# Optimization experiments

Measured on AMD Instinct MI355X. Metric: run time of the kernel, lower is better.

Reference implementation:

```python
import jax, jax.numpy as jnp
import numpy as np

N, H, V = 8192, 1024, 32000
IGNORE_INDEX = -100
LABEL_SMOOTHING = 0.0
LOGIT_SCALE = 1.0


def setup_inputs() -> dict:
    key = jax.random.key(0)
    k1, k2, k3 = jax.random.split(key, 3)
    x = jax.random.normal(k1, (N, H), dtype=jnp.float32)
    weight = jax.random.normal(k2, (V, H), dtype=jnp.float32) * 0.02
    bias = jnp.zeros((V,), dtype=jnp.float32)
    target = jax.random.randint(k3, (N,), 0, V, dtype=jnp.int64)
    return {"x": x, "weight": weight, "bias": bias, "target": target}


def reference(x, weight, bias, target):
    # logits: [N, V]; fused kernel never materializes this fully, but math is identical
    logits = (x @ weight.T + bias) * LOGIT_SCALE
    lse = jax.nn.logsumexp(logits.astype(jnp.float32), axis=-1)  # [N]
    valid = target != IGNORE_INDEX
    safe_t = jnp.where(valid, target, 0)
    tgt_logit = jnp.take_along_axis(logits, safe_t[:, None], axis=-1)[:, 0]
    loss_i = lse - tgt_logit
    if LABEL_SMOOTHING > 0:
        eps = LABEL_SMOOTHING / V
        z = (-eps * logits).sum(-1)
        loss_i = loss_i * (1.0 - LABEL_SMOOTHING) + (z + LABEL_SMOOTHING * lse)
    loss_i = jnp.where(valid, loss_i, 0.0)
    total = jnp.maximum(valid.sum(), 1)
    # reduction == 'mean': each per-token loss divided by total, then summed
    return loss_i.sum() / total
```

## Files before the change

kernel.cpp:

```cpp
#include <hip/hip_runtime.h>
#include <math.h>

typedef int    intx8    __attribute__((ext_vector_type(8)));
typedef float  floatx16 __attribute__((ext_vector_type(16)));

#define N_ROWS 8192
#define H_DIM  1024
#define V_DIM  32000
#define V_PAD  32768
#define IGNORE_INDEX (-100)

#define S_SPLITS 16
#define TILES_PER_SPLIT 16
#define BM 256
#define BN 128
#define KSTEPS 16
#define TOTAL_STEPS (TILES_PER_SPLIT * KSTEPS)
#define BBUF (4 * 128 * 16)

#define LOG2E 1.4426950408889634f
#define LN2   0.6931471805599453f

__global__ __launch_bounds__(256) void convert_fp8(const float* __restrict__ in,
                                                   unsigned char* __restrict__ out,
                                                   int Rstride, float scale) {
  const int r = blockIdx.x * 256 + threadIdx.x;
  const int u = blockIdx.y;
  const float4* src = (const float4*)(in + (size_t)r * H_DIM + u * 16);
  uint4 res;
#pragma unroll
  for (int j = 0; j < 4; ++j) {
    const float4 v = src[j];
    int p = __builtin_amdgcn_cvt_pk_fp8_f32(v.x * scale, v.y * scale, 0, false);
    p = __builtin_amdgcn_cvt_pk_fp8_f32(v.z * scale, v.w * scale, p, true);
    ((int*)&res)[j] = p;
  }
  *(uint4*)(out + ((size_t)u * Rstride + r) * 16) = res;
}

__global__ __launch_bounds__(256) void pad_bias(const float* __restrict__ bias,
                                                float* __restrict__ biasp) {
  const int i = blockIdx.x * 256 + threadIdx.x;
  biasp[i] = (i < V_DIM) ? bias[i] * LOG2E : -1e30f;
}


typedef union { intx8 v; uint4 q[2]; } afrag;

#define BDMA(T) do {                                                                     \
    const int _t = (T);                                                                  \
    const int _ub = (_t & 15) * 4;                                                       \
    const int _n0 = (sidx * TILES_PER_SPLIT + (_t >> 4)) * BN;                           \
    unsigned char* _d = smB + ((_t & 1) ? BBUF : 0);                                     \
    _Pragma("unroll")                                                                    \
    for (int _j = 0; _j < 2; ++_j) {                                                     \
      const int _c = _j * 4 + w, _u = _c >> 1, _rb = _c & 1;                             \
      __builtin_amdgcn_global_load_lds(                                                  \
          (const __attribute__((address_space(1))) void*)(wsb +                          \
              ((size_t)(_ub + _u) * V_PAD + _n0 + _rb * 64 + lane) * 16),                \
          (__attribute__((address_space(3))) void*)(_d + ((_u * 128 + _rb * 64 + lane) * 16)), \
          16, 0, 0);                                                                     \
    }                                                                                    \
  } while (0)

#define ALD(T, DST) do {                                                                 \
    const int _u2 = ((T) & 15) * 4 + half * 2;                                           \
    DST[0].q[0] = *(const uint4*)(xs + (((size_t)(_u2    ) * N_ROWS + arow0) * 16));     \
    DST[0].q[1] = *(const uint4*)(xs + (((size_t)(_u2 + 1) * N_ROWS + arow0) * 16));     \
    DST[1].q[0] = *(const uint4*)(xs + (((size_t)(_u2    ) * N_ROWS + arow1) * 16));     \
    DST[1].q[1] = *(const uint4*)(xs + (((size_t)(_u2 + 1) * N_ROWS + arow1) * 16));     \
  } while (0)

#define STEP(T, AU, AL) do {                                                             \
    const int _st = (T);                                                                 \
    __syncthreads();       \
    if (_st + 1 < TOTAL_STEPS) {                                                         \
      BDMA(_st + 1);                                                                     \
      ALD(_st + 1, AL);                                                                  \
    }                                                                                    \
    const unsigned char* _pB = smB + ((_st & 1) ? BBUF : 0);                             \
    afrag b[4];                                                                          \
    const int _ua = half * 2;                                                            \
    _Pragma("unroll")                                                                    \
    for (int nb = 0; nb < 4; ++nb) {                                                     \
      b[nb].q[0] = *(const uint4*)(_pB + ((_ua * 128 + nb * 32 + l31) * 16));            \
      b[nb].q[1] = *(const uint4*)(_pB + (((_ua + 1) * 128 + nb * 32 + l31) * 16));      \
    }                                                                                    \
    __builtin_amdgcn_s_setprio(1);                                                       \
    _Pragma("unroll")                                                                    \
    for (int mb = 0; mb < 2; ++mb)                                                       \
      _Pragma("unroll")                                                                  \
      for (int nb = 0; nb < 4; ++nb)                                                     \
        acc[mb][nb] = __builtin_amdgcn_mfma_scale_f32_32x32x64_f8f6f4(                   \
            AU[mb].v, b[nb].v, acc[mb][nb],                                              \
            0, 0,                                                  \
            0, 0x7F7F7F7F,                                            \
            0, 0x7F7F7F7F);                                           \
    __builtin_amdgcn_s_setprio(0);                                                       \
  } while (0)

__global__ __launch_bounds__(256, 2) void flce_main(const unsigned char* __restrict__ xs,
                                                    const unsigned char* __restrict__ wsb,
                                                    const float* __restrict__ biasp,
                                                    float* __restrict__ partials) {
  __shared__ __align__(16) unsigned char smB[2 * BBUF];

  const int tid  = threadIdx.x;
  const int lane = tid & 63;
  const int w    = tid >> 6;
  const int l31  = lane & 31;
  const int half = lane >> 5;
  const int wr   = w * 64;

  const int hw     = blockIdx.y * 32 + blockIdx.x;
  const int rowblk = hw >> 4;
  const int sidx   = ((hw & 7) << 1) | ((hw >> 3) & 1);
  const int row0   = rowblk * BM;

  const size_t arow0 = (size_t)(row0 + wr + l31);
  const size_t arow1 = arow0 + 32;

  float l_state[32];
#pragma unroll
  for (int i = 0; i < 32; ++i) l_state[i] = 0.f;

  afrag aE[2], aO[2];

  BDMA(0);
  ALD(0, aE);

#pragma unroll 1
  for (int ct = 0; ct < TILES_PER_SPLIT; ++ct) {
    floatx16 acc[2][4];
#pragma unroll
    for (int mb = 0; mb < 2; ++mb)
#pragma unroll
      for (int nb = 0; nb < 4; ++nb)
#pragma unroll
        for (int i = 0; i < 16; ++i) acc[mb][nb][i] = 0.f;

#pragma unroll 1
    for (int ks2 = 0; ks2 < 8; ++ks2) {
      const int st0 = ct * KSTEPS + ks2 * 2;
      STEP(st0,     aE, aO);
      STEP(st0 + 1, aO, aE);
    }

    const int n0 = (sidx * TILES_PER_SPLIT + ct) * BN;
    float bnb[4];
#pragma unroll
    for (int nb = 0; nb < 4; ++nb) bnb[nb] = biasp[n0 + nb * 32 + l31];
#pragma unroll
    for (int mb = 0; mb < 2; ++mb)
#pragma unroll
      for (int r = 0; r < 16; ++r) {
        float s = exp2f(acc[mb][0][r] + bnb[0]) + exp2f(acc[mb][1][r] + bnb[1])
                + exp2f(acc[mb][2][r] + bnb[2]) + exp2f(acc[mb][3][r] + bnb[3]);
        l_state[mb * 16 + r] += s;
      }
  }

#pragma unroll
  for (int s = 0; s < 32; ++s) {
    float v = l_state[s];
#pragma unroll
    for (int off = 1; off < 32; off <<= 1) v += __shfl_xor(v, off, 64);
    l_state[s] = v;
  }

  if (l31 == 0) {
#pragma unroll
    for (int s = 0; s < 32; ++s) {
      const int mb = s >> 4, r = s & 15;
      const int row = wr + mb * 32 + 4 * half + (r & 3) + 8 * (r >> 2);
      partials[(size_t)(row0 + row) * S_SPLITS + sidx] = l_state[s];
    }
  }
}

__global__ __launch_bounds__(256) void tgt_kernel(const float* __restrict__ x,
                                                  const float* __restrict__ wgt,
                                                  const float* __restrict__ bias,
                                                  const int* __restrict__ target,
                                                  float* __restrict__ tgt_logit) {
  const int r = blockIdx.x * 4 + (threadIdx.x >> 6);
  const int lane = threadIdx.x & 63;
  const int t = target[r];
  const int tt = (t == IGNORE_INDEX) ? 0 : t;
  const float4* xr = (const float4*)(x + (size_t)r * H_DIM);
  const float4* wr = (const float4*)(wgt + (size_t)tt * H_DIM);
  float acc = 0.f;
#pragma unroll
  for (int i = 0; i < 4; ++i) {
    const float4 a = xr[lane + i * 64];
    const float4 b = wr[lane + i * 64];
    acc += a.x * b.x + a.y * b.y + a.z * b.z + a.w * b.w;
  }
#pragma unroll
  for (int off = 32; off >= 1; off >>= 1) acc += __shfl_xor(acc, off, 64);
  if (lane == 0) tgt_logit[r] = acc + bias[tt];
}

__global__ __launch_bounds__(256) void loss_rows(const float* __restrict__ partials,
                                                 const float* __restrict__ tgt_logit,
                                                 const int* __restrict__ target,
                                                 float* __restrict__ bsums) {
  const int r = blockIdx.x * 256 + threadIdx.x;
  float l = 0.f;
#pragma unroll
  for (int s = 0; s < S_SPLITS; ++s) l += partials[(size_t)r * S_SPLITS + s];
  const float lse = LN2 * __log2f(l);
  const bool valid = (target[r] != IGNORE_INDEX);
  float loss = valid ? (lse - tgt_logit[r]) : 0.f;
  float cnt  = valid ? 1.f : 0.f;
  const int lane = threadIdx.x & 63;
  const int w = threadIdx.x >> 6;
#pragma unroll
  for (int off = 32; off >= 1; off >>= 1) {
    loss += __shfl_xor(loss, off, 64);
    cnt  += __shfl_xor(cnt, off, 64);
  }
  __shared__ float sl[4], sc[4];
  if (lane == 0) { sl[w] = loss; sc[w] = cnt; }
  __syncthreads();
  if (threadIdx.x == 0) {
    float S = 0.f, C = 0.f;
    for (int i = 0; i < 4; ++i) { S += sl[i]; C += sc[i]; }
    bsums[blockIdx.x] = S;
    bsums[32 + blockIdx.x] = C;
  }
}

__global__ void finalize(const float* __restrict__ bsums, float* __restrict__ out) {
  const int t = threadIdx.x;
  float s = (t < 32) ? bsums[t] : 0.f;
  float c = (t < 32) ? bsums[32 + t] : 0.f;
#pragma unroll
  for (int off = 32; off >= 1; off >>= 1) {
    s += __shfl_xor(s, off, 64);
    c += __shfl_xor(c, off, 64);
  }
  if (t == 0) out[0] = s / fmaxf(c, 1.f);
}

extern "C" void kernel_launch(void* const* d_in, const int* in_sizes, int n_in,
                              void* d_out, int out_size, void* d_ws, size_t ws_size,
                              hipStream_t stream) {
  const float* x    = (const float*)d_in[0];
  const float* wgt  = (const float*)d_in[1];
  const float* bias = (const float*)d_in[2];
  const int*   tgt  = (const int*)d_in[3];
  float* out = (float*)d_out;

  char* ws = (char*)d_ws;
  const size_t XS8 = (size_t)N_ROWS * H_DIM;
  const size_t WS8 = (size_t)V_PAD * H_DIM;
  const size_t BP  = (size_t)V_PAD * 4;
  const size_t PB  = (size_t)N_ROWS * S_SPLITS * 4;
  unsigned char* xs8 = (unsigned char*)ws;
  unsigned char* ws8 = (unsigned char*)(ws + XS8);
  float* biasp    = (float*)(ws + XS8 + WS8);
  float* partials = (float*)(ws + XS8 + WS8 + BP);
  float* tgt_lg   = (float*)(ws + XS8 + WS8 + BP + PB);
  float* bsums    = (float*)(ws + XS8 + WS8 + BP + PB + (size_t)N_ROWS * 4);

  convert_fp8<<<dim3(N_ROWS / 256, H_DIM / 16), 256, 0, stream>>>(x, xs8, N_ROWS, LOG2E);
  convert_fp8<<<dim3(V_DIM / 256, H_DIM / 16), 256, 0, stream>>>(wgt, ws8, V_PAD, 1.0f);
  pad_bias<<<V_PAD / 256, 256, 0, stream>>>(bias, biasp);
  tgt_kernel<<<N_ROWS / 4, 256, 0, stream>>>(x, wgt, bias, tgt, tgt_lg);
  flce_main<<<dim3(N_ROWS / BM, S_SPLITS), 256, 0, stream>>>(xs8, ws8, biasp, partials);
  loss_rows<<<N_ROWS / 256, 256, 0, stream>>>(partials, tgt_lg, tgt, bsums);
  finalize<<<1, 64, 0, stream>>>(bsums, out);
}
```

Baseline: 555.0 us.

## Deepen K-step to 128, split MFMA halves around barrier, stage bias in LDS

The main GEMM loop now handles two 64-wide K chunks per step. The B tile buffer is doubled, and the A fragment for the next step is loaded between the two MFMA halves, with a mid-step barrier, so load latency overlaps compute. Per-tile bias values are preloaded into LDS once by async copy instead of read from global memory each tile. The block-index swizzle is replaced with plain grid mapping. The fp8 convert kernel is also remapped so each thread reads contiguous row chunks for better coalescing, at the cost of more LDS use and a possible loss of L2 locality from dropping the swizzle.

```diff
diff --git a/kernel.cpp b/kernel.cpp
--- a/kernel.cpp
+++ b/kernel.cpp
@@ -14,9 +14,9 @@
 #define TILES_PER_SPLIT 16
 #define BM 256
 #define BN 128
-#define KSTEPS 16
+#define KSTEPS 8
 #define TOTAL_STEPS (TILES_PER_SPLIT * KSTEPS)
-#define BBUF (4 * 128 * 16)
+#define BBUF (8 * 128 * 16)
 
 #define LOG2E 1.4426950408889634f
 #define LN2   0.6931471805599453f
@@ -24,9 +24,9 @@
 __global__ __launch_bounds__(256) void convert_fp8(const float* __restrict__ in,
                                                    unsigned char* __restrict__ out,
                                                    int Rstride, float scale) {
-  const int r = blockIdx.x * 256 + threadIdx.x;
-  const int u = blockIdx.y;
-  const float4* src = (const float4*)(in + (size_t)r * H_DIM + u * 16);
+  const int row = blockIdx.x * 4 + (threadIdx.x >> 6);
+  const int u   = threadIdx.x & 63;
+  const float4* src = (const float4*)(in + (size_t)row * H_DIM + u * 16);
   uint4 res;
 #pragma unroll
   for (int j = 0; j < 4; ++j) {
@@ -35,7 +35,7 @@
     p = __builtin_amdgcn_cvt_pk_fp8_f32(v.z * scale, v.w * scale, p, true);
     ((int*)&res)[j] = p;
   }
-  *(uint4*)(out + ((size_t)u * Rstride + r) * 16) = res;
+  *(uint4*)(out + ((size_t)u * Rstride + row) * 16) = res;
 }
 
 __global__ __launch_bounds__(256) void pad_bias(const float* __restrict__ bias,
@@ -45,58 +45,85 @@
 }
 
 
-typedef union { intx8 v; uint4 q[2]; } afrag;
+typedef union { intx8 v; uint4 q[2]; } frag;
 
 #define BDMA(T) do {                                                                     \
     const int _t = (T);                                                                  \
-    const int _ub = (_t & 15) * 4;                                                       \
-    const int _n0 = (sidx * TILES_PER_SPLIT + (_t >> 4)) * BN;                           \
+    const int _tub = (_t & 7) * 8;                                                       \
+    const int _n0 = (sidx * TILES_PER_SPLIT + (_t >> 3)) * BN;                           \
     unsigned char* _d = smB + ((_t & 1) ? BBUF : 0);                                     \
     _Pragma("unroll")                                                                    \
-    for (int _j = 0; _j < 2; ++_j) {                                                     \
+    for (int _j = 0; _j < 4; ++_j) {                                                     \
       const int _c = _j * 4 + w, _u = _c >> 1, _rb = _c & 1;                             \
       __builtin_amdgcn_global_load_lds(                                                  \
           (const __attribute__((address_space(1))) void*)(wsb +                          \
-              ((size_t)(_ub + _u) * V_PAD + _n0 + _rb * 64 + lane) * 16),                \
+              ((size_t)(_tub + _u) * V_PAD + _n0 + _rb * 64 + lane) * 16),               \
           (__attribute__((address_space(3))) void*)(_d + ((_u * 128 + _rb * 64 + lane) * 16)), \
           16, 0, 0);                                                                     \
     }                                                                                    \
   } while (0)
 
-#define ALD(T, DST) do {                                                                 \
-    const int _u2 = ((T) & 15) * 4 + half * 2;                                           \
-    DST[0].q[0] = *(const uint4*)(xs + (((size_t)(_u2    ) * N_ROWS + arow0) * 16));     \
-    DST[0].q[1] = *(const uint4*)(xs + (((size_t)(_u2 + 1) * N_ROWS + arow0) * 16));     \
-    DST[1].q[0] = *(const uint4*)(xs + (((size_t)(_u2    ) * N_ROWS + arow1) * 16));     \
-    DST[1].q[1] = *(const uint4*)(xs + (((size_t)(_u2 + 1) * N_ROWS + arow1) * 16));     \
-  } while (0)
-
-#define STEP(T, AU, AL) do {                                                             \
+#define STEP(T, AK0, AK0N) do {                                                          \
     const int _st = (T);                                                                 \
-    __syncthreads();       \
+    const int _ub = (_st & 7) * 8;                                                       \
+    __syncthreads();            \
+                                 \
+                 \
+    frag aK1[2];                                                                         \
+    {                                                                                    \
+      const size_t _u1 = (size_t)(_ub + 4 + half2);                                      \
+      aK1[0].q[0] = *(const uint4*)(xs + ((_u1 * N_ROWS + arow0) * 16));                 \
+      aK1[0].q[1] = *(const uint4*)(xs + (((_u1 + 1) * N_ROWS + arow0) * 16));           \
+      aK1[1].q[0] = *(const uint4*)(xs + ((_u1 * N_ROWS + arow1) * 16));                 \
+      aK1[1].q[1] = *(const uint4*)(xs + (((_u1 + 1) * N_ROWS + arow1) * 16));           \
+    }                                                                                    \
+    if (_st + 1 < TOTAL_STEPS) BDMA(_st + 1);           \
+    const unsigned char* _pB = smB + ((_st & 1) ? BBUF : 0);                             \
+           \
+    {                                                                                    \
+      frag b[4];                                                                         \
+      _Pragma("unroll")                                                                  \
+      for (int nb = 0; nb < 4; ++nb) {                                                   \
+        b[nb].q[0] = *(const uint4*)(_pB + (((half2    ) * 128 + nb * 32 + l31) * 16));  \
+        b[nb].q[1] = *(const uint4*)(_pB + (((half2 + 1) * 128 + nb * 32 + l31) * 16));  \
+      }                                                                                  \
+      __builtin_amdgcn_s_setprio(1);                                                     \
+      _Pragma("unroll")                                                                  \
+      for (int mb = 0; mb < 2; ++mb)                                                     \
+        _Pragma("unroll")                                                                \
+        for (int nb = 0; nb < 4; ++nb)                                                   \
+          acc[mb][nb] = __builtin_amdgcn_mfma_scale_f32_32x32x64_f8f6f4(                 \
+              AK0[mb].v, b[nb].v, acc[mb][nb],                                           \
+              0, 0, 0, 0x7F7F7F7F, 0, 0x7F7F7F7F);                                       \
+      __builtin_amdgcn_s_setprio(0);                                                     \
+    }                                                                                    \
+    __builtin_amdgcn_s_barrier();         \
+                                   \
     if (_st + 1 < TOTAL_STEPS) {                                                         \
-      BDMA(_st + 1);                                                                     \
-      ALD(_st + 1, AL);                                                                  \
-    }                                                                                    \
-    const unsigned char* _pB = smB + ((_st & 1) ? BBUF : 0);                             \
-    afrag b[4];                                                                          \
-    const int _ua = half * 2;                                                            \
-    _Pragma("unroll")                                                                    \
-    for (int nb = 0; nb < 4; ++nb) {                                                     \
-      b[nb].q[0] = *(const uint4*)(_pB + ((_ua * 128 + nb * 32 + l31) * 16));            \
-      b[nb].q[1] = *(const uint4*)(_pB + (((_ua + 1) * 128 + nb * 32 + l31) * 16));      \
-    }                                                                                    \
-    __builtin_amdgcn_s_setprio(1);                                                       \
-    _Pragma("unroll")                                                                    \
-    for (int mb = 0; mb < 2; ++mb)                                                       \
+      const size_t _u0 = (size_t)((((_st + 1) & 7) * 8) + half2);                        \
+      AK0N[0].q[0] = *(const uint4*)(xs + ((_u0 * N_ROWS + arow0) * 16));                \
+      AK0N[0].q[1] = *(const uint4*)(xs + (((_u0 + 1) * N_ROWS + arow0) * 16));          \
+      AK0N[1].q[0] = *(const uint4*)(xs + ((_u0 * N_ROWS + arow1) * 16));                \
+      AK0N[1].q[1] = *(const uint4*)(xs + (((_u0 + 1) * N_ROWS + arow1) * 16));          \
+    }                                                                                    \
+                      \
+    {                                                                                    \
+      frag b[4];                                                                         \
       _Pragma("unroll")                                                                  \
-      for (int nb = 0; nb < 4; ++nb)                                                     \
-        acc[mb][nb] = __builtin_amdgcn_mfma_scale_f32_32x32x64_f8f6f4(                   \
-            AU[mb].v, b[nb].v, acc[mb][nb],                                              \
-            0, 0,                                                  \
-            0, 0x7F7F7F7F,                                            \
-            0, 0x7F7F7F7F);                                           \
-    __builtin_amdgcn_s_setprio(0);                                                       \
+      for (int nb = 0; nb < 4; ++nb) {                                                   \
+        b[nb].q[0] = *(const uint4*)(_pB + (((4 + half2) * 128 + nb * 32 + l31) * 16));  \
+        b[nb].q[1] = *(const uint4*)(_pB + (((5 + half2) * 128 + nb * 32 + l31) * 16));  \
+      }                                                                                  \
+      __builtin_amdgcn_s_setprio(1);                                                     \
+      _Pragma("unroll")                                                                  \
+      for (int mb = 0; mb < 2; ++mb)                                                     \
+        _Pragma("unroll")                                                                \
+        for (int nb = 0; nb < 4; ++nb)                                                   \
+          acc[mb][nb] = __builtin_amdgcn_mfma_scale_f32_32x32x64_f8f6f4(                 \
+              aK1[mb].v, b[nb].v, acc[mb][nb],                                           \
+              0, 0, 0, 0x7F7F7F7F, 0, 0x7F7F7F7F);                                       \
+      __builtin_amdgcn_s_setprio(0);                                                     \
+    }                                                                                    \
   } while (0)
 
 __global__ __launch_bounds__(256, 2) void flce_main(const unsigned char* __restrict__ xs,
@@ -104,18 +131,17 @@
                                                     const float* __restrict__ biasp,
                                                     float* __restrict__ partials) {
   __shared__ __align__(16) unsigned char smB[2 * BBUF];
+  __shared__ __align__(16) float sbias[TILES_PER_SPLIT * BN];
 
   const int tid  = threadIdx.x;
   const int lane = tid & 63;
   const int w    = tid >> 6;
   const int l31  = lane & 31;
   const int half = lane >> 5;
+  const int half2 = half * 2;
   const int wr   = w * 64;
-
-  const int hw     = blockIdx.y * 32 + blockIdx.x;
-  const int rowblk = hw >> 4;
-  const int sidx   = ((hw & 7) << 1) | ((hw >> 3) & 1);
-  const int row0   = rowblk * BM;
+  const int row0 = blockIdx.x * BM;
+  const int sidx = blockIdx.y;
 
   const size_t arow0 = (size_t)(row0 + wr + l31);
   const size_t arow1 = arow0 + 32;
@@ -124,10 +150,24 @@
 #pragma unroll
   for (int i = 0; i < 32; ++i) l_state[i] = 0.f;
 
-  afrag aE[2], aO[2];
-
+#pragma unroll
+  for (int j = 0; j < 2; ++j) {
+    const int c = j * 4 + w;
+    __builtin_amdgcn_global_load_lds(
+        (const __attribute__((address_space(1))) void*)(biasp +
+            (size_t)sidx * (TILES_PER_SPLIT * BN) + c * 256 + lane * 4),
+        (__attribute__((address_space(3))) void*)(sbias + c * 256 + lane * 4),
+        16, 0, 0);
+  }
   BDMA(0);
-  ALD(0, aE);
+  frag aK0E[2], aK0O[2];
+  {
+    const size_t _u0 = (size_t)half2;
+    aK0E[0].q[0] = *(const uint4*)(xs + ((_u0 * N_ROWS + arow0) * 16));
+    aK0E[0].q[1] = *(const uint4*)(xs + (((_u0 + 1) * N_ROWS + arow0) * 16));
+    aK0E[1].q[0] = *(const uint4*)(xs + ((_u0 * N_ROWS + arow1) * 16));
+    aK0E[1].q[1] = *(const uint4*)(xs + (((_u0 + 1) * N_ROWS + arow1) * 16));
+  }
 
 #pragma unroll 1
   for (int ct = 0; ct < TILES_PER_SPLIT; ++ct) {
@@ -140,16 +180,15 @@
         for (int i = 0; i < 16; ++i) acc[mb][nb][i] = 0.f;
 
 #pragma unroll 1
-    for (int ks2 = 0; ks2 < 8; ++ks2) {
+    for (int ks2 = 0; ks2 < 4; ++ks2) {
       const int st0 = ct * KSTEPS + ks2 * 2;
-      STEP(st0,     aE, aO);
-      STEP(st0 + 1, aO, aE);
+      STEP(st0,     aK0E, aK0O);
+      STEP(st0 + 1, aK0O, aK0E);
     }
 
-    const int n0 = (sidx * TILES_PER_SPLIT + ct) * BN;
     float bnb[4];
 #pragma unroll
-    for (int nb = 0; nb < 4; ++nb) bnb[nb] = biasp[n0 + nb * 32 + l31];
+    for (int nb = 0; nb < 4; ++nb) bnb[nb] = sbias[ct * BN + nb * 32 + l31];
 #pragma unroll
     for (int mb = 0; mb < 2; ++mb)
 #pragma unroll
@@ -264,8 +303,8 @@
   float* tgt_lg   = (float*)(ws + XS8 + WS8 + BP + PB);
   float* bsums    = (float*)(ws + XS8 + WS8 + BP + PB + (size_t)N_ROWS * 4);
 
-  convert_fp8<<<dim3(N_ROWS / 256, H_DIM / 16), 256, 0, stream>>>(x, xs8, N_ROWS, LOG2E);
-  convert_fp8<<<dim3(V_DIM / 256, H_DIM / 16), 256, 0, stream>>>(wgt, ws8, V_PAD, 1.0f);
+  convert_fp8<<<N_ROWS / 4, 256, 0, stream>>>(x, xs8, N_ROWS, LOG2E);
+  convert_fp8<<<V_DIM / 4, 256, 0, stream>>>(wgt, ws8, V_PAD, 1.0f);
   pad_bias<<<V_PAD / 256, 256, 0, stream>>>(bias, biasp);
   tgt_kernel<<<N_ROWS / 4, 256, 0, stream>>>(x, wgt, bias, tgt, tgt_lg);
   flce_main<<<dim3(N_ROWS / BM, S_SPLITS), 256, 0, stream>>>(xs8, ws8, biasp, partials);
```

Result: slower. 1.430 ms (+157.6%).
